# Optimization experiments

Hardware: AMD Instinct MI355X
Metric: run time of the kernel (lower is better)

## Reference

```python
import jax, jax.numpy as jnp
import numpy as np

F = 32          # final_feature_size
S = 256         # coordinate stride for key packing (coords < 251, offsets +-1)
SENT = 2 ** 30  # sentinel key > any real packed key
DELTAS = [dx * S * S + dy * S + dz
          for dx in (-1, 0, 1) for dy in (-1, 0, 1) for dz in (-1, 0, 1)]  # 27 kernel offsets


def setup_inputs() -> dict:
    rng = np.random.default_rng(0)
    T, per_frame, B, Npts = 16, 40000, 2, 400000
    # --- history sweep voxels: coords [t, x, y, z], t = global frame id ---
    t = np.repeat(np.arange(T, dtype=np.int32), per_frame)
    xyz = rng.integers(1, 251, size=(T * per_frame, 3), dtype=np.int32)
    keys = ((t.astype(np.int64) * S + xyz[:, 0]) * S + xyz[:, 1]) * S + xyz[:, 2]
    _, idx = np.unique(keys, return_index=True)  # ME quantization dedup
    t, xyz = t[idx], xyz[idx]
    n = t.shape[0]
    history_coordinates = np.concatenate([t[:, None], xyz], axis=1).astype(np.int32)
    history_batches = (t // (T // B)).astype(np.int32)  # scene id per voxel
    history_features = rng.standard_normal((n, 1)).astype(np.float32)
    # --- current scan query points ---
    b = rng.integers(0, B, size=Npts).astype(np.int32)
    qxyz = rng.integers(1, 251, size=(Npts, 3), dtype=np.int32)
    curr_coords = np.concatenate([b[:, None], qxyz], axis=1).astype(np.int32)
    points = np.concatenate([b[:, None].astype(np.float32),
                             qxyz.astype(np.float32),
                             rng.standard_normal((Npts, 1)).astype(np.float32)], axis=1)
    # --- params ---
    W_bb = (rng.standard_normal((27, 1, F)) * (2.0 / 27) ** 0.5).astype(np.float32)
    W_conv = (rng.standard_normal((27, F, F)) * (1.0 / (27 * F)) ** 0.5).astype(np.float32)
    return {
        'history_features': jnp.asarray(history_features),
        'points': jnp.asarray(points),
        'W_bb': jnp.asarray(W_bb),
        'W_conv': jnp.asarray(W_conv),
        'history_coordinates': jnp.asarray(history_coordinates),
        'history_batches': jnp.asarray(history_batches),
        'curr_coords': jnp.asarray(curr_coords),
    }


def pack4(c):
    c = c.astype(jnp.int32)
    return ((c[:, 0] * S + c[:, 1]) * S + c[:, 2]) * S + c[:, 3]


def sparse_conv(sorted_keys, table_feats, out_keys, W):
    """Minkowski-style sparse conv: gather neighbor at each of 27 offsets, matmul, scatter-add."""
    n = sorted_keys.shape[0]
    out = jnp.zeros((out_keys.shape[0], W.shape[2]), table_feats.dtype)
    for i, d in enumerate(DELTAS):
        nk = out_keys + d
        pos = jnp.clip(jnp.searchsorted(sorted_keys, nk), 0, n - 1)
        valid = (sorted_keys[pos] == nk)[:, None]
        g = jnp.where(valid, table_feats[pos], 0.0)
        out = out + g @ W[i]
    return out


def reference(history_features, points, W_bb, W_conv,
              history_coordinates, history_batches, curr_coords):
    n = history_features.shape[0]
    # ---- history backbone (stand-in: one sparse 3x3x3 conv, 1->F, time col as batch) ----
    keys_h = pack4(history_coordinates)
    order = jnp.argsort(keys_h)
    bb = sparse_conv(keys_h[order], history_features[order], keys_h, W_bb)  # [n, F]
    # ---- MinkowskiMaxPooling kernel [1000,1,1,1]: max over time per (b,x,y,z) ----
    pool_coords = jnp.concatenate([history_batches[:, None], history_coordinates[:, 1:4]], axis=1)
    keys_p = pack4(pool_coords)
    uk, inv = jnp.unique(keys_p, return_inverse=True, size=n, fill_value=SENT)  # sorted
    pooled = jax.ops.segment_max(bb, inv, num_segments=n)                        # [n, F]
    # ---- current_conv evaluated at (unique) query voxels, then slice back to points ----
    keys_q = pack4(curr_coords)
    m = keys_q.shape[0]
    uq, qinv = jnp.unique(keys_q, return_inverse=True, size=m, fill_value=SENT)
    conv_q = sparse_conv(uk, pooled, uq, W_conv)  # [m, F]
    ofield = conv_q[qinv]                          # TensorField slice: per-point features
    # ---- mode='update_point_features', preserve_feature==3 ----
    return jnp.concatenate([points[:, :4], ofield], axis=1)  # [Npts, 4+F]
```

## Files before the change

kernel.cpp:

```cpp
#include <hip/hip_runtime.h>
#include <stdint.h>


#define TPB 256
#define SCAN_WPT 8
typedef unsigned long long u64;
typedef unsigned int u32;
typedef unsigned short u16;

__device__ __forceinline__ u32 trans16(float x) {
    u32 b = __float_as_uint(x);
    u32 bf = (b + 0x7FFFu + ((b >> 16) & 1u)) >> 16;
    return ((bf & 0x8000u) ? (~bf) : (bf | 0x8000u)) & 0xFFFFu;
}
__device__ __forceinline__ float detrans16(u32 u) {
    u32 orig = (u & 0x8000u) ? (u & 0x7FFFu) : ((~u) & 0xFFFFu);
    return __uint_as_float(orig << 16);
}

__global__ void build_bitmaps_kernel(const int4* __restrict__ hc,
                                     const int* __restrict__ hb,
                                     int n,
                                     u64* __restrict__ hist_bm,
                                     u64* __restrict__ pool_bm,
                                     u64* __restrict__ multi_bm) {
    int j = blockIdx.x * blockDim.x + threadIdx.x;
    if (j >= n) return;
    int4 c = hc[j];
    int key = ((c.x * 256 + c.y) * 256 + c.z) * 256 + c.w;
    atomicOr(&hist_bm[key >> 6], 1ull << (key & 63));
    int pk = ((hb[j] * 256 + c.y) * 256 + c.z) * 256 + c.w;
    u64 bit = 1ull << (pk & 63);
    u64 old = atomicOr(&pool_bm[pk >> 6], bit);
    if (old & bit) atomicOr(&multi_bm[pk >> 6], bit);
}

__global__ void scan_sum_kernel(const u64* __restrict__ bm, u32* __restrict__ bsum) {
    __shared__ u32 s[TPB];
    int t = threadIdx.x;
    size_t base = ((size_t)blockIdx.x * TPB + t) * SCAN_WPT;
    u32 acc = 0;
#pragma unroll
    for (int i = 0; i < SCAN_WPT; i++) acc += __popcll(bm[base + i]);
    s[t] = acc; __syncthreads();
    for (int off = TPB / 2; off > 0; off >>= 1) {
        if (t < off) s[t] += s[t + off];
        __syncthreads();
    }
    if (t == 0) bsum[blockIdx.x] = s[0];
}

__global__ void scan_partials_kernel(u32* __restrict__ bsum, int count) {
    __shared__ u32 s[TPB];
    int t = threadIdx.x;
    int wpt = count >> 8;
    u32 v[8]; u32 acc = 0;
    for (int i = 0; i < wpt; i++) { v[i] = bsum[t * wpt + i]; acc += v[i]; }
    s[t] = acc; __syncthreads();
    for (int off = 1; off < TPB; off <<= 1) {
        u32 x = (t >= off) ? s[t - off] : 0;
        __syncthreads();
        s[t] += x;
        __syncthreads();
    }
    u32 run = s[t] - acc;
    for (int i = 0; i < wpt; i++) { bsum[t * wpt + i] = run; run += v[i]; }
}

__global__ void scan_apply_kernel(const u64* __restrict__ bm,
                                  const u32* __restrict__ bsum,
                                  u32* __restrict__ rank) {
    __shared__ u32 s[TPB];
    int t = threadIdx.x;
    size_t base = ((size_t)blockIdx.x * TPB + t) * SCAN_WPT;
    u32 pc[SCAN_WPT]; u32 acc = 0;
#pragma unroll
    for (int i = 0; i < SCAN_WPT; i++) { pc[i] = __popcll(bm[base + i]); acc += pc[i]; }
    s[t] = acc; __syncthreads();
    for (int off = 1; off < TPB; off <<= 1) {
        u32 x = (t >= off) ? s[t - off] : 0;
        __syncthreads();
        s[t] += x;
        __syncthreads();
    }
    u32 run = bsum[blockIdx.x] + s[t] - acc;
#pragma unroll
    for (int i = 0; i < SCAN_WPT; i++) { rank[base + i] = run; run += pc[i]; }
}

__global__ void bb_pool_kernel(const int4* __restrict__ hc,
                               const int* __restrict__ hb,
                               const float* __restrict__ hf,
                               const float* __restrict__ Wbb,
                               int n,
                               const u64* __restrict__ hist_bm,
                               const u32* __restrict__ hist_rank,
                               const u64* __restrict__ pool_bm,
                               const u32* __restrict__ pool_rank,
                               const u64* __restrict__ multi_bm,
                               u32* __restrict__ pooled) {
    int p = (blockIdx.x * blockDim.x + threadIdx.x) >> 5;
    if (p >= n) return;
    int lane = threadIdx.x & 63;
    int hb32 = lane & 32;
    int f = lane & 31;

    int4 c = hc[p];
    int key = ((c.x * 256 + c.y) * 256 + c.z) * 256 + c.w;
    int pk = ((hb[p] * 256 + c.y) * 256 + c.z) * 256 + c.w;

    u64 pword = pool_bm[pk >> 6];
    u32 prank = pool_rank[pk >> 6];
    u64 mword = multi_bm[pk >> 6];

    float fv = 0.f;
    bool hit = false;
    if (f < 27) {
        int t1 = f / 9, rem = f - t1 * 9, t2 = rem / 3, t3 = rem - t2 * 3;
        int nk = key + (t1 - 1) * 65536 + (t2 - 1) * 256 + (t3 - 1);
        u64 word = hist_bm[nk >> 6];
        u32 rk   = hist_rank[nk >> 6];
        if ((word >> (nk & 63)) & 1ull) {
            u32 r = rk + (u32)__popcll(word & ((1ull << (nk & 63)) - 1ull));
            fv = hf[r];
            hit = true;
        }
    }
    unsigned long long bal = __ballot(hit);
    u32 mymask = (u32)(bal >> hb32);

    float acc = 0.f;
    while (mymask) {
        int b = __ffs(mymask) - 1;
        mymask &= mymask - 1;
        float fb = __shfl(fv, hb32 + b);
        acc = fmaf(fb, Wbb[b * 32 + f], acc);
    }

    int bit = pk & 63;
    int slot = (int)(prank + (u32)__popcll(pword & ((1ull << bit) - 1ull)));
    bool multi = (mword >> bit) & 1ull;

    u32 tv = trans16(acc);
    u32 packed = tv | (((u32)__shfl_down((int)tv, 1)) << 16);
    if ((f & 1) == 0) {
        u32* addr = pooled + (size_t)slot * 16 + (f >> 1);
        if (!multi) {
            *addr = packed;
        } else {
            u32 oldv = *addr;
            while (true) {
                u32 lo = max(oldv & 0xFFFFu, packed & 0xFFFFu);
                u32 hi = max(oldv >> 16, packed >> 16);
                u32 mx = lo | (hi << 16);
                if (mx == oldv) break;
                u32 prev = atomicCAS(addr, oldv, mx);
                if (prev == oldv) break;
                oldv = prev;
            }
        }
    }
}

__global__ void query_kernel(const int4* __restrict__ qc,
                             const float* __restrict__ pts,
                             const float* __restrict__ Wc,
                             int m,
                             const u64* __restrict__ pool_bm,
                             const u32* __restrict__ pool_rank,
                             const u16* __restrict__ pooled16,
                             float* __restrict__ out) {
    int p = (blockIdx.x * blockDim.x + threadIdx.x) >> 5;
    if (p >= m) return;
    int lane = threadIdx.x & 63;
    int hb32 = lane & 32;
    int f = lane & 31;

    int4 c = qc[p];
    int qk = ((c.x * 256 + c.y) * 256 + c.z) * 256 + c.w;

    int slotL = -1;
    if (f < 27) {
        int t1 = f / 9, rem = f - t1 * 9, t2 = rem / 3, t3 = rem - t2 * 3;
        int nk = qk + (t1 - 1) * 65536 + (t2 - 1) * 256 + (t3 - 1);
        u64 word = pool_bm[nk >> 6];
        u32 rk   = pool_rank[nk >> 6];
        if ((word >> (nk & 63)) & 1ull)
            slotL = (int)(rk + (u32)__popcll(word & ((1ull << (nk & 63)) - 1ull)));
    }
    unsigned long long bal = __ballot(slotL >= 0);
    u32 mymask = (u32)(bal >> hb32);

    float acc = 0.f;
    while (mymask) {
        int b = __ffs(mymask) - 1;
        mymask &= mymask - 1;
        int slot = __shfl(slotL, hb32 + b);
        float pv = detrans16(pooled16[(size_t)slot * 32 + f]);
        const float* W = Wc + b * 1024 + f;
#pragma unroll
        for (int k = 0; k < 32; k++) {
            float pk_ = __shfl(pv, hb32 + k);
            acc = fmaf(pk_, W[k * 32], acc);
        }
    }

    out[(size_t)p * 36 + 4 + f] = acc;
    if (f < 4) out[(size_t)p * 36 + f] = pts[p * 5 + f];
}

extern "C" void kernel_launch(void* const* d_in, const int* in_sizes, int n_in,
                              void* d_out, int out_size, void* d_ws, size_t ws_size,
                              hipStream_t stream) {
    const float* hfeat   = (const float*)d_in[0];
    const float* pts     = (const float*)d_in[1];
    const float* Wbb     = (const float*)d_in[2];
    const float* Wconv   = (const float*)d_in[3];
    const int4*  hcoords = (const int4*)d_in[4];
    const int*   hbatch  = (const int*)d_in[5];
    const int4*  qcoords = (const int4*)d_in[6];
    int n = in_sizes[0];
    int m = in_sizes[1] / 5;

    const int NW_H = 1 << 22;
    const int NW_P = 1 << 19;
    const int GB_H = NW_H / (TPB * SCAN_WPT);
    const int GB_P = NW_P / (TPB * SCAN_WPT);

    char* w = (char*)d_ws;
    char* zbase = w;
    u32* pooled       = (u32*)w;       w += (size_t)n * 64;
    u64* hist_bm      = (u64*)w;       w += (size_t)NW_H * 8;
    u64* pool_bm      = (u64*)w;       w += (size_t)NW_P * 8;
    u64* multi_bm     = (u64*)w;       w += (size_t)NW_P * 8;
    size_t zbytes = (size_t)(w - zbase);
    u32* hist_rank    = (u32*)w;       w += (size_t)NW_H * 4;
    u32* pool_rank    = (u32*)w;       w += (size_t)NW_P * 4;
    u32* bsum_h       = (u32*)w;       w += (size_t)GB_H * 4;
    u32* bsum_p       = (u32*)w;

    hipMemsetAsync(zbase, 0x00, zbytes, stream);

    int gb_n   = (n + TPB - 1) / TPB;
    int gb_n32 = (int)(((long long)n * 32 + TPB - 1) / TPB);
    int gb_m32 = (int)(((long long)m * 32 + TPB - 1) / TPB);

    build_bitmaps_kernel<<<gb_n, TPB, 0, stream>>>(hcoords, hbatch, n,
                                                   hist_bm, pool_bm, multi_bm);
    scan_sum_kernel<<<GB_H, TPB, 0, stream>>>(hist_bm, bsum_h);
    scan_partials_kernel<<<1, TPB, 0, stream>>>(bsum_h, GB_H);
    scan_apply_kernel<<<GB_H, TPB, 0, stream>>>(hist_bm, bsum_h, hist_rank);
    scan_sum_kernel<<<GB_P, TPB, 0, stream>>>(pool_bm, bsum_p);
    scan_partials_kernel<<<1, TPB, 0, stream>>>(bsum_p, GB_P);
    scan_apply_kernel<<<GB_P, TPB, 0, stream>>>(pool_bm, bsum_p, pool_rank);
    bb_pool_kernel<<<gb_n32, TPB, 0, stream>>>(hcoords, hbatch, hfeat, Wbb, n,
                                               hist_bm, hist_rank,
                                               pool_bm, pool_rank, multi_bm, pooled);
    query_kernel<<<gb_m32, TPB, 0, stream>>>(qcoords, pts, Wconv, m,
                                             pool_bm, pool_rank,
                                             (const u16*)pooled, (float*)d_out);
}
```

Baseline: 285.0 us.

## Fetch z-neighbor triples from one bitmap window and zero only multi-hit pool rows

Both the backbone and query kernels now look up the 3 z-adjacent neighbors with a single 64-bit bitmap word (plus a second word at word boundaries), using 9 lanes instead of 27 separate bitmap/rank lookups. This cuts scattered bitmap and rank memory traffic. The memset of the whole pooled buffer (n*64 bytes) is replaced by a small kernel that zeroes only the rows written by several voxels, which need an initial value for the atomic max. The cost is an extra launch that scans the multi bitmap, plus more branchy per-lane logic.

```diff
diff --git a/kernel.cpp b/kernel.cpp
--- a/kernel.cpp
+++ b/kernel.cpp
@@ -86,6 +86,25 @@
     u32 run = bsum[blockIdx.x] + s[t] - acc;
 #pragma unroll
     for (int i = 0; i < SCAN_WPT; i++) { rank[base + i] = run; run += pc[i]; }
+}
+
+__global__ void zero_multi_kernel(const u64* __restrict__ multi_bm,
+                                  const u64* __restrict__ pool_bm,
+                                  const u32* __restrict__ pool_rank,
+                                  u32* __restrict__ pooled) {
+    int wI = blockIdx.x * blockDim.x + threadIdx.x;
+    u64 mw = multi_bm[wI];
+    if (!mw) return;
+    u64 pw = pool_bm[wI];
+    u32 rb = pool_rank[wI];
+    while (mw) {
+        int b = __ffsll((long long)mw) - 1;
+        mw &= mw - 1;
+        u32 slot = rb + (u32)__popcll(pw & ((1ull << b) - 1ull));
+        u32* row = pooled + (size_t)slot * 16;
+#pragma unroll
+        for (int i = 0; i < 16; i++) row[i] = 0u;
+    }
 }
 
 __global__ void bb_pool_kernel(const int4* __restrict__ hc,
@@ -113,28 +132,44 @@
     u32 prank = pool_rank[pk >> 6];
     u64 mword = multi_bm[pk >> 6];
 
-    float fv = 0.f;
-    bool hit = false;
-    if (f < 27) {
-        int t1 = f / 9, rem = f - t1 * 9, t2 = rem / 3, t3 = rem - t2 * 3;
-        int nk = key + (t1 - 1) * 65536 + (t2 - 1) * 256 + (t3 - 1);
-        u64 word = hist_bm[nk >> 6];
-        u32 rk   = hist_rank[nk >> 6];
-        if ((word >> (nk & 63)) & 1ull) {
-            u32 r = rk + (u32)__popcll(word & ((1ull << (nk & 63)) - 1ull));
-            fv = hf[r];
-            hit = true;
-        }
-    }
-    unsigned long long bal = __ballot(hit);
-    u32 mymask = (u32)(bal >> hb32);
+    u32 bits = 0;
+    float fv0 = 0.f, fv1 = 0.f, fv2 = 0.f;
+    if (f < 9) {
+        int t1 = f / 3, t2 = f - t1 * 3;
+        int a = key + (t1 - 1) * 65536 + (t2 - 1) * 256 - 1;
+        int q = a >> 6, s = a & 63;
+        u64 w0 = hist_bm[q];
+        u64 w1 = 0;
+        if (s >= 62) w1 = hist_bm[q + 1];
+        u64 win = w0 >> s;
+        if (s >= 62) win |= w1 << (64 - s);
+        bits = (u32)win & 7u;
+        if (bits) {
+#pragma unroll
+            for (int j = 0; j < 3; j++) if ((bits >> j) & 1u) {
+                int kj = a + j;
+                int wq = kj >> 6, wb = kj & 63;
+                u64 wd = (wq == q) ? w0 : w1;
+                u32 r = hist_rank[wq] + (u32)__popcll(wd & ((1ull << wb) - 1ull));
+                float v = hf[r];
+                if (j == 0) fv0 = v; else if (j == 1) fv1 = v; else fv2 = v;
+            }
+        }
+    }
+
+    unsigned long long bal = __ballot(bits != 0);
+    u32 lm = (u32)(bal >> hb32) & 0x1FFu;
 
     float acc = 0.f;
-    while (mymask) {
-        int b = __ffs(mymask) - 1;
-        mymask &= mymask - 1;
-        float fb = __shfl(fv, hb32 + b);
-        acc = fmaf(fb, Wbb[b * 32 + f], acc);
+    while (lm) {
+        int l = __ffs(lm) - 1;
+        lm &= lm - 1;
+        u32 b3 = (u32)__shfl((int)bits, hb32 + l);
+#pragma unroll
+        for (int j = 0; j < 3; j++) if ((b3 >> j) & 1u) {
+            float fb = __shfl(j == 0 ? fv0 : j == 1 ? fv1 : fv2, hb32 + l);
+            acc = fmaf(fb, Wbb[(l * 3 + j) * 32 + f], acc);
+        }
     }
 
     int bit = pk & 63;
@@ -179,29 +214,49 @@
     int4 c = qc[p];
     int qk = ((c.x * 256 + c.y) * 256 + c.z) * 256 + c.w;
 
-    int slotL = -1;
-    if (f < 27) {
-        int t1 = f / 9, rem = f - t1 * 9, t2 = rem / 3, t3 = rem - t2 * 3;
-        int nk = qk + (t1 - 1) * 65536 + (t2 - 1) * 256 + (t3 - 1);
-        u64 word = pool_bm[nk >> 6];
-        u32 rk   = pool_rank[nk >> 6];
-        if ((word >> (nk & 63)) & 1ull)
-            slotL = (int)(rk + (u32)__popcll(word & ((1ull << (nk & 63)) - 1ull)));
-    }
-    unsigned long long bal = __ballot(slotL >= 0);
-    u32 mymask = (u32)(bal >> hb32);
+    u32 bits = 0;
+    int sl0 = -1, sl1 = -1, sl2 = -1;
+    if (f < 9) {
+        int t1 = f / 3, t2 = f - t1 * 3;
+        int a = qk + (t1 - 1) * 65536 + (t2 - 1) * 256 - 1;
+        int q = a >> 6, s = a & 63;
+        u64 w0 = pool_bm[q];
+        u64 w1 = 0;
+        if (s >= 62) w1 = pool_bm[q + 1];
+        u64 win = w0 >> s;
+        if (s >= 62) win |= w1 << (64 - s);
+        bits = (u32)win & 7u;
+        if (bits) {
+#pragma unroll
+            for (int j = 0; j < 3; j++) if ((bits >> j) & 1u) {
+                int kj = a + j;
+                int wq = kj >> 6, wb = kj & 63;
+                u64 wd = (wq == q) ? w0 : w1;
+                int s_ = (int)(pool_rank[wq] +
+                               (u32)__popcll(wd & ((1ull << wb) - 1ull)));
+                if (j == 0) sl0 = s_; else if (j == 1) sl1 = s_; else sl2 = s_;
+            }
+        }
+    }
+
+    unsigned long long bal = __ballot(bits != 0);
+    u32 lm = (u32)(bal >> hb32) & 0x1FFu;
 
     float acc = 0.f;
-    while (mymask) {
-        int b = __ffs(mymask) - 1;
-        mymask &= mymask - 1;
-        int slot = __shfl(slotL, hb32 + b);
-        float pv = detrans16(pooled16[(size_t)slot * 32 + f]);
-        const float* W = Wc + b * 1024 + f;
-#pragma unroll
-        for (int k = 0; k < 32; k++) {
-            float pk_ = __shfl(pv, hb32 + k);
-            acc = fmaf(pk_, W[k * 32], acc);
+    while (lm) {
+        int l = __ffs(lm) - 1;
+        lm &= lm - 1;
+        u32 b3 = (u32)__shfl((int)bits, hb32 + l);
+#pragma unroll
+        for (int j = 0; j < 3; j++) if ((b3 >> j) & 1u) {
+            int slot = __shfl(j == 0 ? sl0 : j == 1 ? sl1 : sl2, hb32 + l);
+            float pv = detrans16(pooled16[(size_t)slot * 32 + f]);
+            const float* W = Wc + (l * 3 + j) * 1024 + f;
+#pragma unroll
+            for (int k = 0; k < 32; k++) {
+                float pk_ = __shfl(pv, hb32 + k);
+                acc = fmaf(pk_, W[k * 32], acc);
+            }
         }
     }
 
@@ -229,11 +284,11 @@
 
     char* w = (char*)d_ws;
     char* zbase = w;
-    u32* pooled       = (u32*)w;       w += (size_t)n * 64;
     u64* hist_bm      = (u64*)w;       w += (size_t)NW_H * 8;
     u64* pool_bm      = (u64*)w;       w += (size_t)NW_P * 8;
     u64* multi_bm     = (u64*)w;       w += (size_t)NW_P * 8;
     size_t zbytes = (size_t)(w - zbase);
+    u32* pooled       = (u32*)w;       w += (size_t)n * 64;
     u32* hist_rank    = (u32*)w;       w += (size_t)NW_H * 4;
     u32* pool_rank    = (u32*)w;       w += (size_t)NW_P * 4;
     u32* bsum_h       = (u32*)w;       w += (size_t)GB_H * 4;
@@ -253,6 +308,8 @@
     scan_sum_kernel<<<GB_P, TPB, 0, stream>>>(pool_bm, bsum_p);
     scan_partials_kernel<<<1, TPB, 0, stream>>>(bsum_p, GB_P);
     scan_apply_kernel<<<GB_P, TPB, 0, stream>>>(pool_bm, bsum_p, pool_rank);
+    zero_multi_kernel<<<NW_P / TPB, TPB, 0, stream>>>(multi_bm, pool_bm,
+                                                      pool_rank, pooled);
     bb_pool_kernel<<<gb_n32, TPB, 0, stream>>>(hcoords, hbatch, hfeat, Wbb, n,
                                                hist_bm, hist_rank,
                                                pool_bm, pool_rank, multi_bm, pooled);
```

Result: slower. 371.1 us (+30.2%).

## Zero only multi-contributor pooled rows instead of memsetting whole pooled buffer

Applied to the files above, without the earlier changes.

Moves the pooled feature buffer out of the memset region and adds a kernel that zeroes only the rows of pooled voxels with multiple contributors, which are the only rows updated by atomic max. This removes a full n*64-byte memset. It also adds launch bounds to the two main kernels and writes query outputs as float2 pairs via a lane shuffle. Correctness relies on single-contributor rows always being fully written by bb_pool, and the zeroing relies on the packed 16-bit encoding mapping zero to the minimum value.

```diff
diff --git a/kernel.cpp b/kernel.cpp
--- a/kernel.cpp
+++ b/kernel.cpp
@@ -88,17 +88,37 @@
     for (int i = 0; i < SCAN_WPT; i++) { rank[base + i] = run; run += pc[i]; }
 }
 
-__global__ void bb_pool_kernel(const int4* __restrict__ hc,
-                               const int* __restrict__ hb,
-                               const float* __restrict__ hf,
-                               const float* __restrict__ Wbb,
-                               int n,
-                               const u64* __restrict__ hist_bm,
-                               const u32* __restrict__ hist_rank,
-                               const u64* __restrict__ pool_bm,
-                               const u32* __restrict__ pool_rank,
-                               const u64* __restrict__ multi_bm,
-                               u32* __restrict__ pooled) {
+__global__ void zero_multi_kernel(const u64* __restrict__ multi_bm,
+                                  const u64* __restrict__ pool_bm,
+                                  const u32* __restrict__ pool_rank,
+                                  u32* __restrict__ pooled) {
+    int wI = blockIdx.x * blockDim.x + threadIdx.x;
+    u64 mw = multi_bm[wI];
+    if (!mw) return;
+    u64 pw = pool_bm[wI];
+    u32 rb = pool_rank[wI];
+    while (mw) {
+        int b = __ffsll((long long)mw) - 1;
+        mw &= mw - 1;
+        u32 slot = rb + (u32)__popcll(pw & ((1ull << b) - 1ull));
+        u32* row = pooled + (size_t)slot * 16;
+#pragma unroll
+        for (int i = 0; i < 16; i++) row[i] = 0u;
+    }
+}
+
+__global__ __launch_bounds__(TPB, 8)
+void bb_pool_kernel(const int4* __restrict__ hc,
+                    const int* __restrict__ hb,
+                    const float* __restrict__ hf,
+                    const float* __restrict__ Wbb,
+                    int n,
+                    const u64* __restrict__ hist_bm,
+                    const u32* __restrict__ hist_rank,
+                    const u64* __restrict__ pool_bm,
+                    const u32* __restrict__ pool_rank,
+                    const u64* __restrict__ multi_bm,
+                    u32* __restrict__ pooled) {
     int p = (blockIdx.x * blockDim.x + threadIdx.x) >> 5;
     if (p >= n) return;
     int lane = threadIdx.x & 63;
@@ -162,14 +182,15 @@
     }
 }
 
-__global__ void query_kernel(const int4* __restrict__ qc,
-                             const float* __restrict__ pts,
-                             const float* __restrict__ Wc,
-                             int m,
-                             const u64* __restrict__ pool_bm,
-                             const u32* __restrict__ pool_rank,
-                             const u16* __restrict__ pooled16,
-                             float* __restrict__ out) {
+__global__ __launch_bounds__(TPB, 8)
+void query_kernel(const int4* __restrict__ qc,
+                  const float* __restrict__ pts,
+                  const float* __restrict__ Wc,
+                  int m,
+                  const u64* __restrict__ pool_bm,
+                  const u32* __restrict__ pool_rank,
+                  const u16* __restrict__ pooled16,
+                  float* __restrict__ out) {
     int p = (blockIdx.x * blockDim.x + threadIdx.x) >> 5;
     if (p >= m) return;
     int lane = threadIdx.x & 63;
@@ -205,7 +226,11 @@
         }
     }
 
-    out[(size_t)p * 36 + 4 + f] = acc;
+    float acc2 = __shfl_down(acc, 1);
+    if ((f & 1) == 0) {
+        float2 st; st.x = acc; st.y = acc2;
+        *(float2*)(out + (size_t)p * 36 + 4 + f) = st;
+    }
     if (f < 4) out[(size_t)p * 36 + f] = pts[p * 5 + f];
 }
 
@@ -229,11 +254,11 @@
 
     char* w = (char*)d_ws;
     char* zbase = w;
-    u32* pooled       = (u32*)w;       w += (size_t)n * 64;
     u64* hist_bm      = (u64*)w;       w += (size_t)NW_H * 8;
     u64* pool_bm      = (u64*)w;       w += (size_t)NW_P * 8;
     u64* multi_bm     = (u64*)w;       w += (size_t)NW_P * 8;
     size_t zbytes = (size_t)(w - zbase);
+    u32* pooled       = (u32*)w;       w += (size_t)n * 64;
     u32* hist_rank    = (u32*)w;       w += (size_t)NW_H * 4;
     u32* pool_rank    = (u32*)w;       w += (size_t)NW_P * 4;
     u32* bsum_h       = (u32*)w;       w += (size_t)GB_H * 4;
@@ -253,6 +278,8 @@
     scan_sum_kernel<<<GB_P, TPB, 0, stream>>>(pool_bm, bsum_p);
     scan_partials_kernel<<<1, TPB, 0, stream>>>(bsum_p, GB_P);
     scan_apply_kernel<<<GB_P, TPB, 0, stream>>>(pool_bm, bsum_p, pool_rank);
+    zero_multi_kernel<<<NW_P / TPB, TPB, 0, stream>>>(multi_bm, pool_bm,
+                                                      pool_rank, pooled);
     bb_pool_kernel<<<gb_n32, TPB, 0, stream>>>(hcoords, hbatch, hfeat, Wbb, n,
                                                hist_bm, hist_rank,
                                                pool_bm, pool_rank, multi_bm, pooled);
```

New measurement: 283.6 us. No clear change (-0.5%).
